# Kernel tuning notes

Hardware: AMD Instinct MI355X
Metric: run time of the kernel (lower is better)

Reference implementation:

```python
import jax, jax.numpy as jnp
import numpy as np

B, N, D, H, L = 4, 256, 512, 8, 3
HD = D // H
K_SPARSE = max(1, int(N * 0.1))  # top-k edges per node
EPS = 1e-5  # torch LayerNorm default


def _mha(x, Wqkv, bqkv, Wo, bo):
    b, n, d = x.shape
    qkv = x @ Wqkv + bqkv
    q, k, v = jnp.split(qkv, 3, axis=-1)
    rs = lambda t: t.reshape(b, n, H, HD).transpose(0, 2, 1, 3)
    q, k, v = rs(q), rs(k), rs(v)
    att = jax.nn.softmax(jnp.einsum('bhqd,bhkd->bhqk', q, k) * (HD ** -0.5), axis=-1)
    out = jnp.einsum('bhqk,bhkd->bhqd', att, v).transpose(0, 2, 1, 3).reshape(b, n, d)
    return out @ Wo + bo


def _ln(x, g, b):
    m = x.mean(-1, keepdims=True)
    v = ((x - m) ** 2).mean(-1, keepdims=True)
    return (x - m) / jnp.sqrt(v + EPS) * g + b


def setup_inputs() -> dict:
    key = jax.random.key(0)
    ks = iter(jax.random.split(key, 32))
    rn = lambda *s: jax.random.normal(next(ks), s, jnp.float32) * 0.02
    return {
        'x': jax.random.normal(next(ks), (B, N, D), jnp.float32),
        'adjacency': jax.random.uniform(next(ks), (B, N, N), jnp.float32),
        'Wqkv': rn(L, D, 3 * D), 'bqkv': rn(L, 3 * D),
        'Wo': rn(L, D, D), 'bo': rn(L, D),
        'Wp1': rn(L - 1, D, D // 2), 'bp1': rn(L - 1, D // 2),
        'Wp2': rn(L - 1, D // 2, D), 'bp2': rn(L - 1, D),
        'Wfuse': rn(L * D, D), 'bfuse': rn(D),
        'ln_g': jnp.ones((D,), jnp.float32), 'ln_b': jnp.zeros((D,), jnp.float32),
        'We1': rn(2 * D, D), 'be1': rn(D), 'We2': rn(D, 1), 'be2': rn(1),
        'Ws_qkv': rn(D, 3 * D), 'bs_qkv': rn(3 * D),
        'Ws_o': rn(D, D), 'bs_o': rn(D),
    }


def reference(x, adjacency, Wqkv, bqkv, Wo, bo, Wp1, bp1, Wp2, bp2, Wfuse, bfuse,
              ln_g, ln_b, We1, be1, We2, be2, Ws_qkv, bs_qkv, Ws_o, bs_o):
    # --- HierarchicalGraphAttention ---
    cur = x
    level_outs = []
    for l in range(L):  # fixed small hierarchy loop
        a = _mha(cur, Wqkv[l], bqkv[l], Wo[l], bo[l])
        level_outs.append(a)
        if l < L - 1:
            p = jax.nn.relu(a @ Wp1[l] + bp1[l]) @ Wp2[l] + bp2[l]
            cur = p.reshape(B, -1, 2, D).mean(axis=2)  # pairwise pooling halves nodes
    # upsample each level back to N nodes (repeat_interleave), fuse
    fused = [jnp.repeat(o, N // o.shape[1], axis=1) for o in level_outs]
    hier = _ln(jax.nn.relu(jnp.concatenate(fused, axis=-1) @ Wfuse + bfuse), ln_g, ln_b)

    # --- SparseGraphOperations: O(N^2) edge scoring + per-row top-k ---
    # cat([x_i, x_j]) @ We1 == x_i @ We1[:D] + x_j @ We1[D:]
    hi = hier @ We1[:D]                      # [B,N,D]
    hj = hier @ We1[D:] + be1                # [B,N,D]
    pre = hi[:, :, None, :] + hj[:, None, :, :]  # [B,N,N,D]
    scores = jax.nn.sigmoid((jax.nn.relu(pre) @ We2 + be2)[..., 0])  # [B,N,N]
    scores = jnp.where(jnp.eye(N, dtype=bool)[None], 0.0, scores)    # i != j only
    _, idx = jax.lax.top_k(scores, K_SPARSE)  # [B,N,K]
    sparse_adj = jnp.zeros((B, N, N), jnp.float32).at[
        jnp.arange(B)[:, None, None], jnp.arange(N)[None, :, None], idx].set(1.0)

    attended = _mha(hier, Ws_qkv, bs_qkv, Ws_o, bs_o)
    return attended, sparse_adj
```

## Files before the change

kernel.cpp:

```cpp
#include <hip/hip_runtime.h>
#include <math.h>


template <int TM, typename ACC>
__global__ __launch_bounds__(256) void gemm_v3(
    const float* __restrict__ A, const float* __restrict__ W,
    const float* __restrict__ bias, float* __restrict__ C,
    int M, int N, int K, int flags, int wmode)
{
    constexpr int RT = TM / 16;
    constexpr int PAD = 4;
    __shared__ ACC As[16][TM + PAD];
    __shared__ ACC Ws[16][64 + PAD];

    const int tid = threadIdx.x;
    const int tx = tid & 15, ty = tid >> 4;
    const int bm = blockIdx.y * TM, bn = blockIdx.x * 64;

    const float* Wp = W;
    const float* bp = bias;
    int wn = N, wcol = bn;
    if (wmode == 1) {
        int seg = (bm >= 1536) ? 2 : (bm >= 1024) ? 1 : 0;
        Wp += (size_t)seg * 262144;
    } else if (wmode == 2) {
        if (bn >= 512) Wp += 262144; else bp = nullptr;
        wn = 512; wcol = bn & 511;
    }

    const int ar = tid >> 3, ac = (tid & 7) << 1;
    const int wr = tid >> 4;
    const int wc = (tid & 15) << 2;

    const float* Aptr = A + (size_t)(bm + ar) * K + ac;
    const float* Wptr = Wp + (size_t)wr * wn + wcol + wc;

    ACC acc[RT][4] = {};
    float ra[2], rw[4];

    {
        float2 v = *(const float2*)Aptr; ra[0] = v.x; ra[1] = v.y;
        float4 w = *(const float4*)Wptr;
        rw[0]=w.x; rw[1]=w.y; rw[2]=w.z; rw[3]=w.w;
    }

    for (int k0 = 0; k0 < K; k0 += 16) {
        if (k0) __syncthreads();
        As[ac + 0][ar] = (ACC)ra[0];
        As[ac + 1][ar] = (ACC)ra[1];
        #pragma unroll
        for (int u = 0; u < 4; ++u) Ws[wr][wc + u] = (ACC)rw[u];
        __syncthreads();

        if (k0 + 16 < K) {
            float2 v = *(const float2*)(Aptr + k0 + 16); ra[0] = v.x; ra[1] = v.y;
            float4 w = *(const float4*)(Wptr + (size_t)(k0 + 16) * wn);
            rw[0]=w.x; rw[1]=w.y; rw[2]=w.z; rw[3]=w.w;
        }

        #pragma unroll
        for (int kk = 0; kk < 16; ++kk) {
            ACC a[RT], w[4];
            #pragma unroll
            for (int i = 0; i < RT; ++i) a[i] = As[kk][ty * RT + i];
            #pragma unroll
            for (int j = 0; j < 4; ++j) w[j] = Ws[kk][tx * 4 + j];
            #pragma unroll
            for (int i = 0; i < RT; ++i)
                #pragma unroll
                for (int j = 0; j < 4; ++j)
                    acc[i][j] += a[i] * w[j];
        }
    }

    #pragma unroll
    for (int j = 0; j < 4; ++j) {
        const int cn = bn + tx * 4 + j;
        const ACC bv = bp ? (ACC)bp[(wmode == 2) ? (cn & 511) : cn] : (ACC)0;
        if (flags & 2) {
            #pragma unroll
            for (int pi = 0; pi < RT / 2; ++pi) {
                ACC f0 = acc[2 * pi][j] + bv;
                ACC f1 = acc[2 * pi + 1][j] + bv;
                if (flags & 1) {
                    f0 = f0 > (ACC)0 ? f0 : (ACC)0;
                    f1 = f1 > (ACC)0 ? f1 : (ACC)0;
                }
                int prow = ((bm + ty * RT) >> 1) + pi;
                C[(size_t)prow * N + cn] = (float)((f0 + f1) * (ACC)0.5);
            }
        } else {
            #pragma unroll
            for (int i = 0; i < RT; ++i) {
                ACC f = acc[i][j] + bv;
                if (flags & 1) f = f > (ACC)0 ? f : (ACC)0;
                C[(size_t)(bm + ty * RT + i) * N + cn] = (float)f;
            }
        }
    }
}

template <int NT>
__global__ __launch_bounds__(256) void attn_v2(
    const float* __restrict__ qkv, float* __restrict__ out, int n)
{
    const int lane = threadIdx.x & 63;
    const int w    = threadIdx.x >> 6;
    const int h = blockIdx.y, b = blockIdx.z;
    const int q0 = blockIdx.x * 16;
    const size_t base = (size_t)b * n * 1536;

    __shared__ float q_lds[16][64];
    __shared__ float kv_lds[64][65];
    __shared__ float p_lds[16][256];

    {
        int r = threadIdx.x >> 4, c4 = (threadIdx.x & 15) << 2;
        float4 v = *(const float4*)(qkv + base + (size_t)(q0 + r) * 1536 + h * 64 + c4);
        q_lds[r][c4 + 0] = v.x; q_lds[r][c4 + 1] = v.y;
        q_lds[r][c4 + 2] = v.z; q_lds[r][c4 + 3] = v.w;
    }

    const int r0 = w * 4;
    const int sr = threadIdx.x >> 2;
    const int sq = threadIdx.x & 3;

    float s[4][NT];

    #pragma unroll
    for (int t = 0; t < NT; ++t) {
        const int j0 = t * 64;
        __syncthreads();
        {
            const float* src = qkv + base + (size_t)(j0 + sr) * 1536 + 512 + h * 64;
            #pragma unroll
            for (int u = 0; u < 4; ++u) {
                int c = u * 4 + sq;
                float4 v = *(const float4*)(src + c * 4);
                kv_lds[sr][c * 4 + 0] = v.x; kv_lds[sr][c * 4 + 1] = v.y;
                kv_lds[sr][c * 4 + 2] = v.z; kv_lds[sr][c * 4 + 3] = v.w;
            }
        }
        __syncthreads();
        float c0 = 0.f, c1 = 0.f, c2 = 0.f, c3 = 0.f;
        #pragma unroll
        for (int d = 0; d < 64; ++d) {
            const float kvv = kv_lds[lane][d];
            c0 = fmaf(q_lds[r0 + 0][d], kvv, c0);
            c1 = fmaf(q_lds[r0 + 1][d], kvv, c1);
            c2 = fmaf(q_lds[r0 + 2][d], kvv, c2);
            c3 = fmaf(q_lds[r0 + 3][d], kvv, c3);
        }
        s[0][t] = c0 * 0.125f; s[1][t] = c1 * 0.125f;
        s[2][t] = c2 * 0.125f; s[3][t] = c3 * 0.125f;
    }

    double inv[4];
    #pragma unroll
    for (int qr = 0; qr < 4; ++qr) {
        float m = s[qr][0];
        #pragma unroll
        for (int t = 1; t < NT; ++t) m = fmaxf(m, s[qr][t]);
        #pragma unroll
        for (int off = 32; off; off >>= 1) m = fmaxf(m, __shfl_xor(m, off));
        double sum = 0.0;
        #pragma unroll
        for (int t = 0; t < NT; ++t) {
            float p = expf(s[qr][t] - m);
            p_lds[r0 + qr][t * 64 + lane] = p;
            sum += (double)p;
        }
        #pragma unroll
        for (int off = 32; off; off >>= 1) sum += __shfl_xor(sum, off);
        inv[qr] = 1.0 / sum;
    }

    float o0 = 0.f, o1 = 0.f, o2 = 0.f, o3 = 0.f;
    #pragma unroll
    for (int t = 0; t < NT; ++t) {
        const int j0 = t * 64;
        __syncthreads();
        {
            const float* src = qkv + base + (size_t)(j0 + sr) * 1536 + 1024 + h * 64;
            #pragma unroll
            for (int u = 0; u < 4; ++u) {
                int c = u * 4 + sq;
                float4 v = *(const float4*)(src + c * 4);
                kv_lds[sr][c * 4 + 0] = v.x; kv_lds[sr][c * 4 + 1] = v.y;
                kv_lds[sr][c * 4 + 2] = v.z; kv_lds[sr][c * 4 + 3] = v.w;
            }
        }
        __syncthreads();
        #pragma unroll
        for (int jl = 0; jl < 64; ++jl) {
            const float vv = kv_lds[jl][lane];
            o0 = fmaf(p_lds[r0 + 0][t * 64 + jl], vv, o0);
            o1 = fmaf(p_lds[r0 + 1][t * 64 + jl], vv, o1);
            o2 = fmaf(p_lds[r0 + 2][t * 64 + jl], vv, o2);
            o3 = fmaf(p_lds[r0 + 3][t * 64 + jl], vv, o3);
        }
    }
    const size_t obase = ((size_t)(b * n + q0 + r0)) * 512 + h * 64 + lane;
    out[obase + 0 * 512] = (float)((double)o0 * inv[0]);
    out[obase + 1 * 512] = (float)((double)o1 * inv[1]);
    out[obase + 2 * 512] = (float)((double)o2 * inv[2]);
    out[obase + 3 * 512] = (float)((double)o3 * inv[3]);
}

__global__ __launch_bounds__(64) void ln3_kernel(
    const float* __restrict__ y, const float* __restrict__ bf,
    const float* __restrict__ g, const float* __restrict__ bta,
    float* __restrict__ out)
{
    const int r = blockIdx.x, lane = threadIdx.x;
    const int b = r >> 8, i = r & 255;
    const float* y0 = y + (size_t)r * 512;
    const float* y1 = y + (size_t)(1024 + b * 128 + (i >> 1)) * 512;
    const float* y2 = y + (size_t)(1536 + b * 64 + (i >> 2)) * 512;
    double v[8];
    double sum = 0.0;
    #pragma unroll
    for (int t = 0; t < 8; ++t) {
        int d = t * 64 + lane;
        double s = (double)y0[d] + (double)y1[d] + (double)y2[d] + (double)bf[d];
        s = s > 0.0 ? s : 0.0;
        v[t] = s; sum += s;
    }
    #pragma unroll
    for (int off = 32; off; off >>= 1) sum += __shfl_xor(sum, off);
    const double mean = sum * (1.0 / 512.0);
    double ss = 0.0;
    #pragma unroll
    for (int t = 0; t < 8; ++t) { double d = v[t] - mean; ss += d * d; }
    #pragma unroll
    for (int off = 32; off; off >>= 1) ss += __shfl_xor(ss, off);
    const double rstd = 1.0 / sqrt(ss * (1.0 / 512.0) + 1e-5);
    #pragma unroll
    for (int t = 0; t < 8; ++t) {
        int d = t * 64 + lane;
        out[(size_t)r * 512 + d] =
            (float)((v[t] - mean) * rstd * (double)g[d] + (double)bta[d]);
    }
}

__global__ __launch_bounds__(256) void scores_v4(
    const float* __restrict__ hibjb, const float* __restrict__ We2,
    const float* __restrict__ be2, float* __restrict__ S)
{
    __shared__ float Hi[128][34];
    __shared__ float Hj[128][34];
    const int b = blockIdx.z;
    const int i0 = blockIdx.y * 32, j0 = blockIdx.x * 32;
    const int tid = threadIdx.x;
    const int tx = tid & 15, ty = tid >> 4;

    const int si = tid >> 3;
    const int sd = (tid & 7) << 2;

    const float* hip = hibjb + (size_t)(b * 256 + i0 + si) * 1024 + sd;
    const float* hjp = hibjb + (size_t)(b * 256 + j0 + si) * 1024 + 512 + sd;

    double a00 = 0.0, a01 = 0.0, a10 = 0.0, a11 = 0.0;

    for (int k0 = 0; k0 < 512; k0 += 128) {
        __syncthreads();
        #pragma unroll
        for (int u = 0; u < 4; ++u) {
            const int dch = u * 32 + sd;
            float4 v = *(const float4*)(hip + k0 + u * 32);
            Hi[dch + 0][si] = v.x; Hi[dch + 1][si] = v.y;
            Hi[dch + 2][si] = v.z; Hi[dch + 3][si] = v.w;
            float4 w = *(const float4*)(hjp + k0 + u * 32);
            Hj[dch + 0][si] = w.x; Hj[dch + 1][si] = w.y;
            Hj[dch + 2][si] = w.z; Hj[dch + 3][si] = w.w;
        }
        __syncthreads();
        #pragma unroll 16
        for (int kk = 0; kk < 128; ++kk) {
            const double wv = (double)We2[k0 + kk];
            const float2 hi = *(const float2*)&Hi[kk][ty * 2];
            const float2 hj = *(const float2*)&Hj[kk][tx * 2];
            a00 += (double)fmaxf(hi.x + hj.x, 0.f) * wv;
            a01 += (double)fmaxf(hi.x + hj.y, 0.f) * wv;
            a10 += (double)fmaxf(hi.y + hj.x, 0.f) * wv;
            a11 += (double)fmaxf(hi.y + hj.y, 0.f) * wv;
        }
    }

    const double bb = (double)be2[0];
    const int gi0 = i0 + ty * 2, gj0 = j0 + tx * 2;
    double zz[2][2] = {{a00, a01}, {a10, a11}};
    #pragma unroll
    for (int ii = 0; ii < 2; ++ii)
        #pragma unroll
        for (int jj = 0; jj < 2; ++jj) {
            double z = zz[ii][jj] + bb;
            float sc_ = (float)(1.0 / (1.0 + exp(-z)));
            if (gi0 + ii == gj0 + jj) sc_ = 0.f;
            S[(size_t)(b * 256 + gi0 + ii) * 256 + gj0 + jj] = sc_;
        }
}

__global__ __launch_bounds__(64) void topk_kernel(
    const float* __restrict__ S, float* __restrict__ out)
{
    const int row = blockIdx.x;
    const int lane = threadIdx.x;
    float v[4]; int sel[4] = {0, 0, 0, 0};
    #pragma unroll
    for (int t = 0; t < 4; ++t) v[t] = S[(size_t)row * 256 + t * 64 + lane];
    for (int it = 0; it < 25; ++it) {
        float bv = v[0]; int bi = lane;
        #pragma unroll
        for (int t = 1; t < 4; ++t) {
            int idx = t * 64 + lane;
            if (v[t] > bv) { bv = v[t]; bi = idx; }
        }
        #pragma unroll
        for (int off = 32; off; off >>= 1) {
            float ov = __shfl_xor(bv, off);
            int   oi = __shfl_xor(bi, off);
            if (ov > bv || (ov == bv && oi < bi)) { bv = ov; bi = oi; }
        }
        if ((bi & 63) == lane) { int t = bi >> 6; sel[t] = 1; v[t] = -INFINITY; }
    }
    #pragma unroll
    for (int t = 0; t < 4; ++t)
        out[(size_t)row * 256 + t * 64 + lane] = (float)sel[t];
}

extern "C" void kernel_launch(void* const* d_in, const int* in_sizes, int n_in,
                              void* d_out, int out_size, void* d_ws, size_t ws_size,
                              hipStream_t stream)
{
    const float* x      = (const float*)d_in[0];
    const float* Wqkv   = (const float*)d_in[2];
    const float* bqkv   = (const float*)d_in[3];
    const float* Wo     = (const float*)d_in[4];
    const float* bo     = (const float*)d_in[5];
    const float* Wp1    = (const float*)d_in[6];
    const float* bp1    = (const float*)d_in[7];
    const float* Wp2    = (const float*)d_in[8];
    const float* bp2    = (const float*)d_in[9];
    const float* Wfuse  = (const float*)d_in[10];
    const float* bfuse  = (const float*)d_in[11];
    const float* ln_g   = (const float*)d_in[12];
    const float* ln_b   = (const float*)d_in[13];
    const float* We1    = (const float*)d_in[14];
    const float* be1    = (const float*)d_in[15];
    const float* We2    = (const float*)d_in[16];
    const float* be2    = (const float*)d_in[17];
    const float* Ws_qkv = (const float*)d_in[18];
    const float* bs_qkv = (const float*)d_in[19];
    const float* Ws_o   = (const float*)d_in[20];
    const float* bs_o   = (const float*)d_in[21];

    float* out_att    = (float*)d_out;
    float* out_sparse = out_att + 4 * 256 * 512;

    float* ws    = (float*)d_ws;
    float* qkvb  = ws;
    float* attnb = qkvb + 1572864;
    float* lvls  = attnb + 524288;
    float* poolb = lvls + 917504;
    float* curb  = poolb + 131072;
    float* hier  = curb + 262144;
    float* hibjb = hier + 524288;
    float* scb   = hibjb + 1048576;

    float* lvl0 = lvls;
    float* lvl1 = lvls + 1024 * 512;
    float* lvl2 = lvls + 1536 * 512;

    auto G32 = [&](const float* A, const float* W, const float* bias, float* C,
                   int M, int N, int K, int flags, int wmode) {
        gemm_v3<32, float><<<dim3(N / 64, M / 32), 256, 0, stream>>>(
            A, W, bias, C, M, N, K, flags, wmode);
    };

    G32(x, Wqkv, bqkv, qkvb, 1024, 1536, 512, 0, 0);
    attn_v2<4><<<dim3(16, 8, 4), 256, 0, stream>>>(qkvb, attnb, 256);
    G32(attnb, Wo, bo, lvl0, 1024, 512, 512, 0, 0);
    G32(lvl0, Wp1, bp1, poolb, 1024, 256, 512, 3, 0);
    G32(poolb, Wp2, bp2, curb, 512, 512, 256, 0, 0);

    G32(curb, Wqkv + 512 * 1536, bqkv + 1536, qkvb, 512, 1536, 512, 0, 0);
    attn_v2<2><<<dim3(8, 8, 4), 256, 0, stream>>>(qkvb, attnb, 128);
    G32(attnb, Wo + 512 * 512, bo + 512, lvl1, 512, 512, 512, 0, 0);
    G32(lvl1, Wp1 + 512 * 256, bp1 + 256, poolb, 512, 256, 512, 3, 0);
    G32(poolb, Wp2 + 256 * 512, bp2 + 512, curb, 256, 512, 256, 0, 0);

    G32(curb, Wqkv + 2 * 512 * 1536, bqkv + 2 * 1536, qkvb, 256, 1536, 512, 0, 0);
    attn_v2<1><<<dim3(4, 8, 4), 256, 0, stream>>>(qkvb, attnb, 64);
    G32(attnb, Wo + 2 * 512 * 512, bo + 2 * 512, lvl2, 256, 512, 512, 0, 0);

    G32(lvls, Wfuse, nullptr, qkvb, 1792, 512, 512, 0, 1);
    ln3_kernel<<<1024, 64, 0, stream>>>(qkvb, bfuse, ln_g, ln_b, hier);

    G32(hier, We1, be1, hibjb, 1024, 1024, 512, 0, 2);
    scores_v4<<<dim3(8, 8, 4), 256, 0, stream>>>(hibjb, We2, be2, scb);
    topk_kernel<<<1024, 64, 0, stream>>>(scb, out_sparse);

    G32(hier, Ws_qkv, bs_qkv, qkvb, 1024, 1536, 512, 0, 0);
    attn_v2<4><<<dim3(16, 8, 4), 256, 0, stream>>>(qkvb, attnb, 256);
    G32(attnb, Ws_o, bs_o, out_att, 1024, 512, 512, 0, 0);
}
```

Before: 413.2 us.

## Fuse hier QKV and edge-projection GEMMs, add 64-row GEMM tiles with vector LDS reads

The two GEMMs that read `hier` (the sparse-attention QKV projection and the We1 edge projections) are merged into one 2560-column GEMM whose output feeds both the scores kernel and the attention kernel, using new stride parameters. A TM=64 GEMM variant is added and used for the larger GEMMs. LDS fragment loads become float4/float2 vector reads, and the accumulation uses explicit fmaf. This removes one launch and one re-read of `hier` and raises arithmetic intensity per tile. The cost is fewer blocks for the big GEMMs and a wider intermediate buffer.

```diff
diff --git a/kernel.cpp b/kernel.cpp
--- a/kernel.cpp
+++ b/kernel.cpp
@@ -2,16 +2,16 @@
 #include <math.h>
 
 
-template <int TM, typename ACC>
-__global__ __launch_bounds__(256) void gemm_v3(
+template <int TM>
+__global__ __launch_bounds__(256) void gemm_v4(
     const float* __restrict__ A, const float* __restrict__ W,
     const float* __restrict__ bias, float* __restrict__ C,
-    int M, int N, int K, int flags, int wmode)
+    int M, int N, int K, int flags, int wmode,
+    const float* __restrict__ W2, const float* __restrict__ bias2)
 {
     constexpr int RT = TM / 16;
-    constexpr int PAD = 4;
-    __shared__ ACC As[16][TM + PAD];
-    __shared__ ACC Ws[16][64 + PAD];
+    __shared__ float As[16][TM + 4];
+    __shared__ float Ws[16][68];
 
     const int tid = threadIdx.x;
     const int tx = tid & 15, ty = tid >> 4;
@@ -23,78 +23,88 @@
     if (wmode == 1) {
         int seg = (bm >= 1536) ? 2 : (bm >= 1024) ? 1 : 0;
         Wp += (size_t)seg * 262144;
-    } else if (wmode == 2) {
-        if (bn >= 512) Wp += 262144; else bp = nullptr;
-        wn = 512; wcol = bn & 511;
-    }
-
-    const int ar = tid >> 3, ac = (tid & 7) << 1;
+    } else if (wmode == 3) {
+        if (bn < 1536)      { wn = 1536; wcol = bn; }
+        else if (bn < 2048) { Wp = W2;           wn = 512; wcol = bn - 1536; bp = nullptr; }
+        else                { Wp = W2 + 262144;  wn = 512; wcol = bn - 2048; bp = bias2; }
+    }
+
+    constexpr int AV = (TM == 64) ? 4 : 2;
+    const int ar = (TM == 64) ? (tid >> 2) : (tid >> 3);
+    const int ac = (TM == 64) ? ((tid & 3) << 2) : ((tid & 7) << 1);
     const int wr = tid >> 4;
     const int wc = (tid & 15) << 2;
 
     const float* Aptr = A + (size_t)(bm + ar) * K + ac;
     const float* Wptr = Wp + (size_t)wr * wn + wcol + wc;
 
-    ACC acc[RT][4] = {};
-    float ra[2], rw[4];
+    float acc[RT][4] = {};
+    float ra[AV], rw[4];
 
     {
-        float2 v = *(const float2*)Aptr; ra[0] = v.x; ra[1] = v.y;
+        if (TM == 64) { float4 v = *(const float4*)Aptr;
+            ra[0]=v.x; ra[1]=v.y; ra[2]=v.z; ra[3]=v.w; }
+        else { float2 v = *(const float2*)Aptr; ra[0]=v.x; ra[1]=v.y; }
         float4 w = *(const float4*)Wptr;
         rw[0]=w.x; rw[1]=w.y; rw[2]=w.z; rw[3]=w.w;
     }
 
     for (int k0 = 0; k0 < K; k0 += 16) {
         if (k0) __syncthreads();
-        As[ac + 0][ar] = (ACC)ra[0];
-        As[ac + 1][ar] = (ACC)ra[1];
-        #pragma unroll
-        for (int u = 0; u < 4; ++u) Ws[wr][wc + u] = (ACC)rw[u];
+        #pragma unroll
+        for (int u = 0; u < AV; ++u) As[ac + u][ar] = ra[u];
+        #pragma unroll
+        for (int u = 0; u < 4; ++u) Ws[wr][wc + u] = rw[u];
         __syncthreads();
 
         if (k0 + 16 < K) {
-            float2 v = *(const float2*)(Aptr + k0 + 16); ra[0] = v.x; ra[1] = v.y;
+            const float* ap = Aptr + k0 + 16;
+            if (TM == 64) { float4 v = *(const float4*)ap;
+                ra[0]=v.x; ra[1]=v.y; ra[2]=v.z; ra[3]=v.w; }
+            else { float2 v = *(const float2*)ap; ra[0]=v.x; ra[1]=v.y; }
             float4 w = *(const float4*)(Wptr + (size_t)(k0 + 16) * wn);
             rw[0]=w.x; rw[1]=w.y; rw[2]=w.z; rw[3]=w.w;
         }
 
         #pragma unroll
         for (int kk = 0; kk < 16; ++kk) {
-            ACC a[RT], w[4];
-            #pragma unroll
-            for (int i = 0; i < RT; ++i) a[i] = As[kk][ty * RT + i];
-            #pragma unroll
-            for (int j = 0; j < 4; ++j) w[j] = Ws[kk][tx * 4 + j];
+            float a[RT];
+            if constexpr (RT == 4) {
+                float4 t = *(const float4*)&As[kk][ty * 4];
+                a[0]=t.x; a[1]=t.y; a[2]=t.z; a[3]=t.w;
+            } else {
+                float2 t = *(const float2*)&As[kk][ty * 2];
+                a[0]=t.x; a[1]=t.y;
+            }
+            float4 tw = *(const float4*)&Ws[kk][tx * 4];
+            float w[4] = {tw.x, tw.y, tw.z, tw.w};
             #pragma unroll
             for (int i = 0; i < RT; ++i)
                 #pragma unroll
                 for (int j = 0; j < 4; ++j)
-                    acc[i][j] += a[i] * w[j];
+                    acc[i][j] = fmaf(a[i], w[j], acc[i][j]);
         }
     }
 
     #pragma unroll
     for (int j = 0; j < 4; ++j) {
         const int cn = bn + tx * 4 + j;
-        const ACC bv = bp ? (ACC)bp[(wmode == 2) ? (cn & 511) : cn] : (ACC)0;
+        const float bv = bp ? bp[wcol + tx * 4 + j] : 0.f;
         if (flags & 2) {
             #pragma unroll
             for (int pi = 0; pi < RT / 2; ++pi) {
-                ACC f0 = acc[2 * pi][j] + bv;
-                ACC f1 = acc[2 * pi + 1][j] + bv;
-                if (flags & 1) {
-                    f0 = f0 > (ACC)0 ? f0 : (ACC)0;
-                    f1 = f1 > (ACC)0 ? f1 : (ACC)0;
-                }
+                float f0 = acc[2 * pi][j] + bv;
+                float f1 = acc[2 * pi + 1][j] + bv;
+                if (flags & 1) { f0 = fmaxf(f0, 0.f); f1 = fmaxf(f1, 0.f); }
                 int prow = ((bm + ty * RT) >> 1) + pi;
-                C[(size_t)prow * N + cn] = (float)((f0 + f1) * (ACC)0.5);
+                C[(size_t)prow * N + cn] = (f0 + f1) * 0.5f;
             }
         } else {
             #pragma unroll
             for (int i = 0; i < RT; ++i) {
-                ACC f = acc[i][j] + bv;
-                if (flags & 1) f = f > (ACC)0 ? f : (ACC)0;
-                C[(size_t)(bm + ty * RT + i) * N + cn] = (float)f;
+                float f = acc[i][j] + bv;
+                if (flags & 1) f = fmaxf(f, 0.f);
+                C[(size_t)(bm + ty * RT + i) * N + cn] = f;
             }
         }
     }
@@ -102,13 +112,13 @@
 
 template <int NT>
 __global__ __launch_bounds__(256) void attn_v2(
-    const float* __restrict__ qkv, float* __restrict__ out, int n)
+    const float* __restrict__ qkv, float* __restrict__ out, int n, int qstride)
 {
     const int lane = threadIdx.x & 63;
     const int w    = threadIdx.x >> 6;
     const int h = blockIdx.y, b = blockIdx.z;
     const int q0 = blockIdx.x * 16;
-    const size_t base = (size_t)b * n * 1536;
+    const size_t base = (size_t)b * n * qstride;
 
     __shared__ float q_lds[16][64];
     __shared__ float kv_lds[64][65];
@@ -116,7 +126,7 @@
 
     {
         int r = threadIdx.x >> 4, c4 = (threadIdx.x & 15) << 2;
-        float4 v = *(const float4*)(qkv + base + (size_t)(q0 + r) * 1536 + h * 64 + c4);
+        float4 v = *(const float4*)(qkv + base + (size_t)(q0 + r) * qstride + h * 64 + c4);
         q_lds[r][c4 + 0] = v.x; q_lds[r][c4 + 1] = v.y;
         q_lds[r][c4 + 2] = v.z; q_lds[r][c4 + 3] = v.w;
     }
@@ -132,7 +142,7 @@
         const int j0 = t * 64;
         __syncthreads();
         {
-            const float* src = qkv + base + (size_t)(j0 + sr) * 1536 + 512 + h * 64;
+            const float* src = qkv + base + (size_t)(j0 + sr) * qstride + 512 + h * 64;
             #pragma unroll
             for (int u = 0; u < 4; ++u) {
                 int c = u * 4 + sq;
@@ -181,7 +191,7 @@
         const int j0 = t * 64;
         __syncthreads();
         {
-            const float* src = qkv + base + (size_t)(j0 + sr) * 1536 + 1024 + h * 64;
+            const float* src = qkv + base + (size_t)(j0 + sr) * qstride + 1024 + h * 64;
             #pragma unroll
             for (int u = 0; u < 4; ++u) {
                 int c = u * 4 + sq;
@@ -244,8 +254,9 @@
 }
 
 __global__ __launch_bounds__(256) void scores_v4(
-    const float* __restrict__ hibjb, const float* __restrict__ We2,
-    const float* __restrict__ be2, float* __restrict__ S)
+    const float* __restrict__ hq, int stride, int off,
+    const float* __restrict__ We2, const float* __restrict__ be2,
+    float* __restrict__ S)
 {
     __shared__ float Hi[128][34];
     __shared__ float Hj[128][34];
@@ -257,8 +268,8 @@
     const int si = tid >> 3;
     const int sd = (tid & 7) << 2;
 
-    const float* hip = hibjb + (size_t)(b * 256 + i0 + si) * 1024 + sd;
-    const float* hjp = hibjb + (size_t)(b * 256 + j0 + si) * 1024 + 512 + sd;
+    const float* hip = hq + (size_t)(b * 256 + i0 + si) * stride + off + sd;
+    const float* hjp = hq + (size_t)(b * 256 + j0 + si) * stride + off + 512 + sd;
 
     double a00 = 0.0, a01 = 0.0, a10 = 0.0, a11 = 0.0;
 
@@ -365,43 +376,49 @@
     float* poolb = lvls + 917504;
     float* curb  = poolb + 131072;
     float* hier  = curb + 262144;
-    float* hibjb = hier + 524288;
-    float* scb   = hibjb + 1048576;
+    float* scb   = hier + 524288;
+    float* qh    = scb + 262144;
 
     float* lvl0 = lvls;
     float* lvl1 = lvls + 1024 * 512;
     float* lvl2 = lvls + 1536 * 512;
 
+    auto G64 = [&](const float* A, const float* W, const float* bias, float* C,
+                   int M, int N, int K, int flags, int wmode,
+                   const float* W2 = nullptr, const float* bias2 = nullptr) {
+        gemm_v4<64><<<dim3(N / 64, M / 64), 256, 0, stream>>>(
+            A, W, bias, C, M, N, K, flags, wmode, W2, bias2);
+    };
     auto G32 = [&](const float* A, const float* W, const float* bias, float* C,
                    int M, int N, int K, int flags, int wmode) {
-        gemm_v3<32, float><<<dim3(N / 64, M / 32), 256, 0, stream>>>(
-            A, W, bias, C, M, N, K, flags, wmode);
+        gemm_v4<32><<<dim3(N / 64, M / 32), 256, 0, stream>>>(
+            A, W, bias, C, M, N, K, flags, wmode, nullptr, nullptr);
     };
 
-    G32(x, Wqkv, bqkv, qkvb, 1024, 1536, 512, 0, 0);
-    attn_v2<4><<<dim3(16, 8, 4), 256, 0, stream>>>(qkvb, attnb, 256);
+    G64(x, Wqkv, bqkv, qkvb, 1024, 1536, 512, 0, 0);
+    attn_v2<4><<<dim3(16, 8, 4), 256, 0, stream>>>(qkvb, attnb, 256, 1536);
     G32(attnb, Wo, bo, lvl0, 1024, 512, 512, 0, 0);
     G32(lvl0, Wp1, bp1, poolb, 1024, 256, 512, 3, 0);
     G32(poolb, Wp2, bp2, curb, 512, 512, 256, 0, 0);
 
-    G32(curb, Wqkv + 512 * 1536, bqkv + 1536, qkvb, 512, 1536, 512, 0, 0);
-    attn_v2<2><<<dim3(8, 8, 4), 256, 0, stream>>>(qkvb, attnb, 128);
+    G64(curb, Wqkv + 512 * 1536, bqkv + 1536, qkvb, 512, 1536, 512, 0, 0);
+    attn_v2<2><<<dim3(8, 8, 4), 256, 0, stream>>>(qkvb, attnb, 128, 1536);
     G32(attnb, Wo + 512 * 512, bo + 512, lvl1, 512, 512, 512, 0, 0);
     G32(lvl1, Wp1 + 512 * 256, bp1 + 256, poolb, 512, 256, 512, 3, 0);
     G32(poolb, Wp2 + 256 * 512, bp2 + 512, curb, 256, 512, 256, 0, 0);
 
     G32(curb, Wqkv + 2 * 512 * 1536, bqkv + 2 * 1536, qkvb, 256, 1536, 512, 0, 0);
-    attn_v2<1><<<dim3(4, 8, 4), 256, 0, stream>>>(qkvb, attnb, 64);
+    attn_v2<1><<<dim3(4, 8, 4), 256, 0, stream>>>(qkvb, attnb, 64, 1536);
     G32(attnb, Wo + 2 * 512 * 512, bo + 2 * 512, lvl2, 256, 512, 512, 0, 0);
 
-    G32(lvls, Wfuse, nullptr, qkvb, 1792, 512, 512, 0, 1);
+    G64(lvls, Wfuse, nullptr, qkvb, 1792, 512, 512, 0, 1);
     ln3_kernel<<<1024, 64, 0, stream>>>(qkvb, bfuse, ln_g, ln_b, hier);
 
-    G32(hier, We1, be1, hibjb, 1024, 1024, 512, 0, 2);
-    scores_v4<<<dim3(8, 8, 4), 256, 0, stream>>>(hibjb, We2, be2, scb);
+    G64(hier, Ws_qkv, bs_qkv, qh, 1024, 2560, 512, 0, 3, We1, be1);
+
+    scores_v4<<<dim3(8, 8, 4), 256, 0, stream>>>(qh, 2560, 1536, We2, be2, scb);
     topk_kernel<<<1024, 64, 0, stream>>>(scb, out_sparse);
 
-    G32(hier, Ws_qkv, bs_qkv, qkvb, 1024, 1536, 512, 0, 0);
-    attn_v2<4><<<dim3(16, 8, 4), 256, 0, stream>>>(qkvb, attnb, 256);
+    attn_v2<4><<<dim3(16, 8, 4), 256, 0, stream>>>(qh, attnb, 256, 2560);
     G32(attnb, Ws_o, bs_o, out_att, 1024, 512, 512, 0, 0);
 }
```

New measurement: 391.1 us. 1.06x faster.
